# Kernel tuning notes

Measured on AMD Instinct MI355X. Metric: run time of the kernel, lower is better.

The kernel has to match this reference:

```python
import jax, jax.numpy as jnp
import numpy as np

GRAPH_SIZE = 100   # nodes per graph (hardcoded reshape in Net.call)
CH = 64            # self.channel
BN_EPS = 1e-3      # keras BatchNormalization default epsilon

N_GRAPHS = 4096
N_NODES = N_GRAPHS * GRAPH_SIZE      # 409600
DEG = 16
N_EDGES = N_NODES * DEG              # 6,553,600


def setup_inputs() -> dict:
    key = jax.random.key(0)
    ks = jax.random.split(key, 12)
    x = jax.random.normal(ks[0], (N_NODES, CH), dtype=jnp.float32)
    # Edges confined within each 100-node graph block (disjoint-union batch).
    receivers = jax.random.randint(ks[1], (N_EDGES,), 0, N_NODES, dtype=jnp.int32)
    block = (receivers // GRAPH_SIZE) * GRAPH_SIZE
    senders = block + jax.random.randint(ks[2], (N_EDGES,), 0, GRAPH_SIZE, dtype=jnp.int32)
    s = lambda fan_in: 1.0 / np.sqrt(fan_in)
    return {
        "x": x,
        "senders": senders,
        "receivers": receivers,
        "W1": jax.random.normal(ks[3], (CH, CH), dtype=jnp.float32) * s(CH),
        "b1": jnp.zeros((CH,), jnp.float32),
        "gamma": jnp.ones((CH,), jnp.float32),
        "beta": jnp.zeros((CH,), jnp.float32),
        "bn_mean": jnp.zeros((CH,), jnp.float32),
        "bn_var": jnp.ones((CH,), jnp.float32),
        "W_d1": jax.random.normal(ks[4], (GRAPH_SIZE * CH, 256), dtype=jnp.float32) * s(GRAPH_SIZE * CH),
        "b_d1": jnp.zeros((256,), jnp.float32),
        "W_d2": jax.random.normal(ks[5], (256, 128), dtype=jnp.float32) * s(256),
        "b_d2": jnp.zeros((128,), jnp.float32),
        "W_d3": jax.random.normal(ks[6], (128, 1), dtype=jnp.float32) * s(128),
        "b_d3": jnp.zeros((1,), jnp.float32),
    }


def reference(x, senders, receivers, W1, b1, gamma, beta, bn_mean, bn_var,
              W_d1, b_d1, W_d2, b_d2, W_d3, b_d3):
    n = x.shape[0]
    # GeneralConv(aggregate='sum'): sum neighbor features, then linear+BN+ELU.
    agg = jax.ops.segment_sum(x[senders], receivers, num_segments=n)  # [N, CH]
    h = agg @ W1 + b1
    h = (h - bn_mean) * (gamma * jax.lax.rsqrt(bn_var + BN_EPS)) + beta
    h = jax.nn.elu(h)
    # reshape [N, CH] -> [N/100, 100*CH] (reshape + Flatten fused)
    h = h.reshape(n // GRAPH_SIZE, GRAPH_SIZE * CH)
    h = jax.nn.relu(h @ W_d1 + b_d1)
    h = jax.nn.relu(h @ W_d2 + b_d2)
    # dropout is identity at inference
    return jax.nn.sigmoid(h @ W_d3 + b_d3)  # [B, 1]
```

## Files before the change

### kernel.cpp

```cpp
#include <hip/hip_runtime.h>
#include <cstdint>
#include <cstddef>

#define GRAPH_SIZE 100
#define N_GRAPHS 4096
#define N_NODES (N_GRAPHS * GRAPH_SIZE)
#define DEG 16
#define N_EDGES (N_NODES * DEG)
#define BN_EPS 1e-3f

#define NB1 1024
#define NPB 400
#define PCHUNK 12800
#define NPWG (N_EDGES / PCHUNK)
#define BSTRIDE 8192
#define ECAP 2304

__global__ __launch_bounds__(256) void count1_kernel(const int* __restrict__ recv,
                                                     unsigned* __restrict__ wg_hist) {
  __shared__ unsigned lh[NB1];
  int tid = threadIdx.x, w = blockIdx.x;
  for (int i = tid; i < NB1; i += 256) lh[i] = 0;
  __syncthreads();
  size_t base = (size_t)w * PCHUNK;
  for (int i = tid; i < PCHUNK; i += 256)
    atomicAdd(&lh[(unsigned)recv[base + i] / NPB], 1u);
  __syncthreads();
  for (int i = tid; i < NB1; i += 256) wg_hist[(size_t)w * NB1 + i] = lh[i];
}

__global__ __launch_bounds__(256) void scan_wg_kernel(unsigned* __restrict__ wg_hist,
                                                      unsigned* __restrict__ gtotal) {
  int b = blockIdx.x * 256 + threadIdx.x;
  unsigned run = 0;
  for (int w = 0; w < NPWG; w++) {
    size_t idx = (size_t)w * NB1 + b;
    unsigned c = wg_hist[idx];
    wg_hist[idx] = run;
    run += c;
  }
  gtotal[b] = run;
}

__global__ __launch_bounds__(256) void scan_bucket_kernel(const unsigned* __restrict__ gtotal,
                                                          unsigned* __restrict__ gbase) {
  __shared__ unsigned tmp[256];
  int tid = threadIdx.x;
  unsigned my[4], s4 = 0;
#pragma unroll
  for (int j = 0; j < 4; j++) { my[j] = gtotal[tid * 4 + j]; s4 += my[j]; }
  tmp[tid] = s4;
  __syncthreads();
  unsigned acc = s4;
  for (int d = 1; d < 256; d <<= 1) {
    unsigned t = (tid >= d) ? tmp[tid - d] : 0;
    __syncthreads();
    acc += t;
    tmp[tid] = acc;
    __syncthreads();
  }
  unsigned run = tmp[tid] - s4;
#pragma unroll
  for (int j = 0; j < 4; j++) { gbase[tid * 4 + j] = run; run += my[j]; }
}

__global__ __launch_bounds__(256) void partition1_kernel(const int* __restrict__ recv,
                                                         const int* __restrict__ send,
                                                         const unsigned* __restrict__ wg_hist,
                                                         const unsigned* __restrict__ gbase,
                                                         unsigned short* __restrict__ midrec) {
  __shared__ unsigned cur[NB1];
  __shared__ unsigned tmp[256];
  __shared__ unsigned stage[PCHUNK];
  int tid = threadIdx.x, w = blockIdx.x;
  size_t base = (size_t)w * PCHUNK;

  for (int i = tid; i < NB1; i += 256) cur[i] = 0;
  __syncthreads();
  for (int i = tid; i < PCHUNK; i += 256)
    atomicAdd(&cur[(unsigned)recv[base + i] / NPB], 1u);
  __syncthreads();

  unsigned my[4], s4 = 0;
#pragma unroll
  for (int j = 0; j < 4; j++) { my[j] = cur[tid * 4 + j]; s4 += my[j]; }
  tmp[tid] = s4;
  __syncthreads();
  unsigned acc = s4;
  for (int d = 1; d < 256; d <<= 1) {
    unsigned t = (tid >= d) ? tmp[tid - d] : 0;
    __syncthreads();
    acc += t;
    tmp[tid] = acc;
    __syncthreads();
  }
  unsigned run = tmp[tid] - s4;
#pragma unroll
  for (int j = 0; j < 4; j++) { cur[tid * 4 + j] = run; run += my[j]; }
  __syncthreads();

  for (int i = tid; i < PCHUNK; i += 256) {
    unsigned r = (unsigned)recv[base + i];
    unsigned s = (unsigned)send[base + i];
    unsigned b = r / NPB;
    unsigned rin = r - b * NPB;
    unsigned gib = rin / 100;
    unsigned rl = rin - gib * 100;
    unsigned sl = s - (s / 100) * 100;
    unsigned pos = atomicAdd(&cur[b], 1u);
    stage[pos] = (b << 16) | (gib << 14) | (sl << 7) | rl;
  }
  __syncthreads();

  const unsigned* wrow = wg_hist + (size_t)w * NB1;
  for (int p = tid; p < PCHUNK; p += 256) {
    unsigned rec = stage[p];
    unsigned b = rec >> 16;
    unsigned start = (b > 0) ? cur[b - 1] : 0;
    unsigned dest = gbase[b] + wrow[b] + ((unsigned)p - start);
    midrec[dest] = (unsigned short)(rec & 0xFFFFu);
  }
}

__global__ __launch_bounds__(256) void sort2_kernel(const unsigned short* __restrict__ midrec,
                                                    const unsigned* __restrict__ gtotal,
                                                    const unsigned* __restrict__ gbase,
                                                    unsigned short* __restrict__ sorted,
                                                    unsigned* __restrict__ noff) {
  __shared__ unsigned short smid[BSTRIDE];
  __shared__ unsigned short dst[BSTRIDE];
  __shared__ unsigned hist[512];
  __shared__ unsigned tmp[256];
  __shared__ unsigned s_ptot;
  int tid = threadIdx.x, b = blockIdx.x;
  unsigned cnt = gtotal[b];
  if (cnt > BSTRIDE) cnt = BSTRIDE;
  unsigned gb = gbase[b];

  for (unsigned i = tid; i < cnt; i += 256) smid[i] = midrec[gb + i];
  hist[tid] = 0; hist[256 + tid] = 0;
  {
    unsigned* d32 = (unsigned*)dst;
    for (int i = tid; i < BSTRIDE / 2; i += 256) d32[i] = 0x19001900u;
  }
  __syncthreads();

  for (unsigned i = tid; i < cnt; i += 256) {
    unsigned rec = smid[i];
    unsigned nib = (rec >> 14) * 100 + (rec & 127u);
    atomicAdd(&hist[nib], 1u);
  }
  __syncthreads();

  unsigned c0 = hist[2 * tid], c1 = hist[2 * tid + 1];
  unsigned p0 = (c0 + 3u) & ~3u, p1 = (c1 + 3u) & ~3u;
  unsigned s2 = p0 + p1;
  tmp[tid] = s2;
  __syncthreads();
  unsigned acc = s2;
  for (int d = 1; d < 256; d <<= 1) {
    unsigned t = (tid >= d) ? tmp[tid - d] : 0;
    __syncthreads();
    acc += t;
    tmp[tid] = acc;
    __syncthreads();
  }
  unsigned pb0 = acc - s2;
  unsigned pb1 = pb0 + p0;
  unsigned obase = (unsigned)b * BSTRIDE;
  int k0 = 2 * tid, k1 = 2 * tid + 1;
  if (k0 <= NPB) noff[(size_t)b * 401 + k0] = obase + pb0;
  if (k1 <= NPB) noff[(size_t)b * 401 + k1] = obase + pb1;
  if (k0 == NPB) s_ptot = pb0;
  __syncthreads();
  hist[k0] = pb0;
  hist[k1] = pb1;
  __syncthreads();

  for (unsigned i = tid; i < cnt; i += 256) {
    unsigned rec = smid[i];
    unsigned nib = (rec >> 14) * 100 + (rec & 127u);
    unsigned pos = atomicAdd(&hist[nib], 1u);
    if (pos < BSTRIDE) dst[pos] = (unsigned short)(((rec >> 7) & 127u) * 64u);
  }
  __syncthreads();

  unsigned ptot = s_ptot;
  if (ptot > BSTRIDE) ptot = BSTRIDE;
  unsigned* o32 = (unsigned*)sorted + (size_t)b * (BSTRIDE / 2);
  unsigned* d32 = (unsigned*)dst;
  for (unsigned i = tid; i < (ptot >> 1); i += 256) o32[i] = d32[i];
}

__global__ __launch_bounds__(256) void aggconv_kernel(
    const float* __restrict__ x, const unsigned* __restrict__ noff,
    const unsigned short* __restrict__ sorted,
    const float* __restrict__ W1, const float* __restrict__ b1,
    const float* __restrict__ gamma, const float* __restrict__ beta,
    const float* __restrict__ bn_mean, const float* __restrict__ bn_var,
    float* __restrict__ h) {
  __shared__ float xs[6464];
  __shared__ unsigned short es[ECAP];
  __shared__ unsigned nof[104];
  int tid = threadIdx.x, lane = tid & 63, wv = tid >> 6;
  int g = blockIdx.x;
  size_t gb64 = (size_t)g * 6400;

  const float4* xsrc = (const float4*)(x + gb64);
  float4* xd = (float4*)xs;
  for (int i = tid; i < 1600; i += 256) xd[i] = xsrc[i];
  if (tid < 64) xs[6400 + tid] = 0.f;

  int b = g >> 2, gib = g & 3;
  size_t base401 = (size_t)b * 401 + (size_t)gib * 100;
  unsigned gbeg = noff[base401];
  unsigned gend = noff[base401 + 100];
  unsigned ecnt = gend - gbeg;
  if (ecnt > ECAP) ecnt = ECAP;
  if (tid <= 100) nof[tid] = noff[base401 + tid] - gbeg;
  {
    const unsigned* s32 = (const unsigned*)sorted + (gbeg >> 1);
    unsigned* e32 = (unsigned*)es;
    for (unsigned i = tid; i < (ecnt >> 1); i += 256) e32[i] = s32[i];
  }
  __syncthreads();

  float accs[25];
#pragma unroll
  for (int J = 0; J < 25; J++) {
    int n = wv + 4 * J;
    unsigned e = nof[n], e1 = nof[n + 1];
    float acc = 0.f;
    for (; e < e1; e += 4) {
      unsigned long long v = *(const unsigned long long*)&es[e];
      acc += xs[((unsigned)v & 0xFFFFu) + lane];
      acc += xs[((unsigned)(v >> 16) & 0xFFFFu) + lane];
      acc += xs[((unsigned)(v >> 32) & 0xFFFFu) + lane];
      acc += xs[(unsigned)(v >> 48) + lane];
    }
    accs[J] = acc;
  }
  __syncthreads();
#pragma unroll
  for (int J = 0; J < 25; J++) xs[(wv + 4 * J) * 64 + lane] = accs[J];
  __syncthreads();

  float w[64];
#pragma unroll
  for (int i = 0; i < 64; i++) w[i] = W1[i * 64 + lane];
  float scale = gamma[lane] * rsqrtf(bn_var[lane] + BN_EPS);
  float mb = bn_mean[lane], bt = beta[lane], bias1 = b1[lane];

#pragma unroll
  for (int J = 0; J < 25; J++) {
    int n = wv + 4 * J;
    float hv = bias1;
#pragma unroll
    for (int q = 0; q < 16; q++) {
      float4 av = *(const float4*)&xs[n * 64 + q * 4];
      hv = fmaf(av.x, w[q * 4 + 0], hv);
      hv = fmaf(av.y, w[q * 4 + 1], hv);
      hv = fmaf(av.z, w[q * 4 + 2], hv);
      hv = fmaf(av.w, w[q * 4 + 3], hv);
    }
    hv = (hv - mb) * scale + bt;
    hv = (hv > 0.f) ? hv : expm1f(hv);
    h[gb64 + (size_t)n * 64 + lane] = hv;
  }
}

#define G2_K 6400
#define G2_SPLIT 8
#define G2_KSLICE (G2_K / G2_SPLIT)
__global__ __launch_bounds__(256) void gemm2_kernel(const float* __restrict__ A,
                                                    const float* __restrict__ B,
                                                    float* __restrict__ Cp) {
  __shared__ float As[16][68];
  __shared__ float Bs[16][256];
  int tid = threadIdx.x;
  int tx = tid & 31;
  int ty = tid >> 5;
  int bm = blockIdx.x * 64;
  int k0base = blockIdx.y * G2_KSLICE;

  float acc[8][8] = {};

  int lm = tid >> 2;
  int lk = (tid & 3) * 4;
  const float* Aptr = A + (size_t)(bm + lm) * G2_K + k0base + lk;
  const float* Bptr = B + (size_t)k0base * 256 + tid;

  float4 apre = *(const float4*)Aptr;
  float bpre[16];
#pragma unroll
  for (int r = 0; r < 16; r++) bpre[r] = Bptr[r * 256];

  const int NT = G2_KSLICE / 16;
  for (int kt = 0; kt < NT; kt++) {
    As[lk + 0][lm] = apre.x;
    As[lk + 1][lm] = apre.y;
    As[lk + 2][lm] = apre.z;
    As[lk + 3][lm] = apre.w;
#pragma unroll
    for (int r = 0; r < 16; r++) Bs[r][tid] = bpre[r];
    __syncthreads();

    if (kt + 1 < NT) {
      apre = *(const float4*)(Aptr + (kt + 1) * 16);
#pragma unroll
      for (int r = 0; r < 16; r++) bpre[r] = Bptr[((kt + 1) * 16 + r) * 256];
    }

#pragma unroll
    for (int kk = 0; kk < 16; kk++) {
      float4 aa = *(const float4*)&As[kk][ty * 8];
      float4 ab = *(const float4*)&As[kk][ty * 8 + 4];
      float a[8] = {aa.x, aa.y, aa.z, aa.w, ab.x, ab.y, ab.z, ab.w};
      float bf[8];
#pragma unroll
      for (int j = 0; j < 8; j++) bf[j] = Bs[kk][tx + 32 * j];
#pragma unroll
      for (int i = 0; i < 8; i++)
#pragma unroll
        for (int j = 0; j < 8; j++) acc[i][j] = fmaf(a[i], bf[j], acc[i][j]);
    }
    __syncthreads();
  }

  float* out = Cp + (size_t)blockIdx.y * N_GRAPHS * 256;
#pragma unroll
  for (int i = 0; i < 8; i++)
#pragma unroll
    for (int j = 0; j < 8; j++)
      out[(size_t)(bm + ty * 8 + i) * 256 + tx + 32 * j] = acc[i][j];
}

__global__ __launch_bounds__(256) void reduce_kernel(const float* __restrict__ Cp,
                                                     const float* __restrict__ bias,
                                                     float* __restrict__ out1) {
  int i = blockIdx.x * 256 + threadIdx.x;
  const size_t S = (size_t)N_GRAPHS * 256;
  float v = bias[i & 255];
#pragma unroll
  for (int s = 0; s < G2_SPLIT; s++) v += Cp[s * S + i];
  out1[i] = fmaxf(v, 0.f);
}

__global__ __launch_bounds__(256) void tail_kernel(const float* __restrict__ out1,
                                                   const float* __restrict__ Wd2,
                                                   const float* __restrict__ bd2,
                                                   const float* __restrict__ Wd3,
                                                   const float* __restrict__ bd3,
                                                   float* __restrict__ out) {
  int lane = threadIdx.x & 63;
  int wave = threadIdx.x >> 6;
  int row = blockIdx.x * 4 + wave;

  const float* in = out1 + (size_t)row * 256;
  float i0 = in[lane];
  float i1 = in[64 + lane];
  float i2 = in[128 + lane];
  float i3 = in[192 + lane];

  float a0 = bd2[lane];
  float a1 = bd2[64 + lane];
#pragma unroll
  for (int i = 0; i < 64; i++) {
    float v0 = __shfl(i0, i);
    a0 = fmaf(v0, Wd2[(i)*128 + lane], a0);
    a1 = fmaf(v0, Wd2[(i)*128 + 64 + lane], a1);
    float v1 = __shfl(i1, i);
    a0 = fmaf(v1, Wd2[(64 + i) * 128 + lane], a0);
    a1 = fmaf(v1, Wd2[(64 + i) * 128 + 64 + lane], a1);
    float v2 = __shfl(i2, i);
    a0 = fmaf(v2, Wd2[(128 + i) * 128 + lane], a0);
    a1 = fmaf(v2, Wd2[(128 + i) * 128 + 64 + lane], a1);
    float v3 = __shfl(i3, i);
    a0 = fmaf(v3, Wd2[(192 + i) * 128 + lane], a0);
    a1 = fmaf(v3, Wd2[(192 + i) * 128 + 64 + lane], a1);
  }
  a0 = fmaxf(a0, 0.f);
  a1 = fmaxf(a1, 0.f);
  float p = a0 * Wd3[lane] + a1 * Wd3[64 + lane];
#pragma unroll
  for (int m = 32; m >= 1; m >>= 1) p += __shfl_xor(p, m);
  if (lane == 0) out[row] = 1.f / (1.f + expf(-(p + bd3[0])));
}

extern "C" void kernel_launch(void* const* d_in, const int* in_sizes, int n_in,
                              void* d_out, int out_size, void* d_ws, size_t ws_size,
                              hipStream_t stream) {
  const float* x        = (const float*)d_in[0];
  const int*   senders  = (const int*)d_in[1];
  const int*   receivers= (const int*)d_in[2];
  const float* W1       = (const float*)d_in[3];
  const float* b1       = (const float*)d_in[4];
  const float* gamma    = (const float*)d_in[5];
  const float* beta     = (const float*)d_in[6];
  const float* bn_mean  = (const float*)d_in[7];
  const float* bn_var   = (const float*)d_in[8];
  const float* W_d1     = (const float*)d_in[9];
  const float* b_d1     = (const float*)d_in[10];
  const float* W_d2     = (const float*)d_in[11];
  const float* b_d2     = (const float*)d_in[12];
  const float* W_d3     = (const float*)d_in[13];
  const float* b_d3     = (const float*)d_in[14];
  float* out = (float*)d_out;

  char* ws = (char*)d_ws;
  float* h = (float*)ws;                 ws += (size_t)N_NODES * 64 * 4;
  char* regB = ws;                       ws += (size_t)NPWG * NB1 * 4;
  unsigned* wg_hist = (unsigned*)regB;
  unsigned* noff    = (unsigned*)regB;
  unsigned* gtotal  = (unsigned*)ws;     ws += NB1 * 4;
  unsigned* gbase   = (unsigned*)ws;     ws += NB1 * 4;
  char* regDE = ws;
  unsigned short* midrec = (unsigned short*)regDE;
  unsigned short* sorted = (unsigned short*)(regDE + (size_t)N_EDGES * 2);
  float* Cp   = (float*)regDE;
  float* out1 = (float*)(regDE + (size_t)G2_SPLIT * N_GRAPHS * 256 * 4);

  count1_kernel<<<NPWG, 256, 0, stream>>>(receivers, wg_hist);
  scan_wg_kernel<<<NB1 / 256, 256, 0, stream>>>(wg_hist, gtotal);
  scan_bucket_kernel<<<1, 256, 0, stream>>>(gtotal, gbase);
  partition1_kernel<<<NPWG, 256, 0, stream>>>(receivers, senders, wg_hist, gbase, midrec);
  sort2_kernel<<<NB1, 256, 0, stream>>>(midrec, gtotal, gbase, sorted, noff);
  aggconv_kernel<<<N_GRAPHS, 256, 0, stream>>>(x, noff, sorted, W1, b1,
                                               gamma, beta, bn_mean, bn_var, h);
  gemm2_kernel<<<dim3(N_GRAPHS / 64, G2_SPLIT), 256, 0, stream>>>(h, W_d1, Cp);
  reduce_kernel<<<(N_GRAPHS * 256) / 256, 256, 0, stream>>>(Cp, b_d1, out1);
  tail_kernel<<<N_GRAPHS / 4, 256, 0, stream>>>(out1, W_d2, b_d2, W_d3, b_d3, out);
}
```

Measured before the change: 627.9 us.

## Run dense-layer GEMM on bf16 MFMA with split hi/lo precision emulation

```diff
diff --git a/kernel.cpp b/kernel.cpp
--- a/kernel.cpp
+++ b/kernel.cpp
@@ -15,6 +15,18 @@
 #define NPWG (N_EDGES / PCHUNK)
 #define BSTRIDE 8192
 #define ECAP 2304
+
+typedef __attribute__((ext_vector_type(8))) unsigned short ushort8;
+typedef __attribute__((ext_vector_type(8))) short short8;
+typedef __attribute__((ext_vector_type(4))) float f32x4;
+
+__device__ __forceinline__ unsigned f2bf(float f) {
+  unsigned u = __float_as_uint(f);
+  return (u + 0x7FFFu + ((u >> 16) & 1u)) >> 16;
+}
+__device__ __forceinline__ float bf2f(unsigned h) {
+  return __uint_as_float(h << 16);
+}
 
 __global__ __launch_bounds__(256) void count1_kernel(const int* __restrict__ recv,
                                                      unsigned* __restrict__ wg_hist) {
@@ -198,7 +210,7 @@
     const float* __restrict__ W1, const float* __restrict__ b1,
     const float* __restrict__ gamma, const float* __restrict__ beta,
     const float* __restrict__ bn_mean, const float* __restrict__ bn_var,
-    float* __restrict__ h) {
+    unsigned short* __restrict__ h_hi, unsigned short* __restrict__ h_lo) {
   __shared__ float xs[6464];
   __shared__ unsigned short es[ECAP];
   __shared__ unsigned nof[104];
@@ -265,74 +277,135 @@
     }
     hv = (hv - mb) * scale + bt;
     hv = (hv > 0.f) ? hv : expm1f(hv);
-    h[gb64 + (size_t)n * 64 + lane] = hv;
-  }
-}
-
-#define G2_K 6400
+    unsigned hi = f2bf(hv);
+    unsigned lo = f2bf(hv - bf2f(hi));
+    size_t idx = gb64 + (size_t)n * 64 + lane;
+    h_hi[idx] = (unsigned short)hi;
+    h_lo[idx] = (unsigned short)lo;
+  }
+}
+
+__global__ __launch_bounds__(256) void wcvt_kernel(const float* __restrict__ W,
+                                                   unsigned short* __restrict__ Bhi,
+                                                   unsigned short* __restrict__ Blo) {
+  __shared__ float sm[64][65];
+  int tid = threadIdx.x;
+  int k0 = blockIdx.x * 64;
+  int n0 = blockIdx.y * 64;
+  for (int i = tid; i < 1024; i += 256) {
+    int r = i >> 4, c4 = i & 15;
+    float4 v = *(const float4*)&W[(size_t)(k0 + r) * 256 + n0 + c4 * 4];
+    sm[r][c4 * 4 + 0] = v.x; sm[r][c4 * 4 + 1] = v.y;
+    sm[r][c4 * 4 + 2] = v.z; sm[r][c4 * 4 + 3] = v.w;
+  }
+  __syncthreads();
+  for (int i = tid; i < 512; i += 256) {
+    int nn = i >> 3, kk = i & 7;
+    ushort8 hi, lo;
+#pragma unroll
+    for (int j = 0; j < 8; j++) {
+      float f = sm[kk * 8 + j][nn];
+      unsigned hb = f2bf(f);
+      hi[j] = (unsigned short)hb;
+      lo[j] = (unsigned short)f2bf(f - bf2f(hb));
+    }
+    size_t o = (size_t)(n0 + nn) * 6400 + k0 + kk * 8;
+    *(ushort8*)&Bhi[o] = hi;
+    *(ushort8*)&Blo[o] = lo;
+  }
+}
+
 #define G2_SPLIT 8
-#define G2_KSLICE (G2_K / G2_SPLIT)
-__global__ __launch_bounds__(256) void gemm2_kernel(const float* __restrict__ A,
-                                                    const float* __restrict__ B,
+#define G2_KSLICE 800
+#define G2_STEPS (G2_KSLICE / 32)
+__global__ __launch_bounds__(256) void gemm2_kernel(const unsigned short* __restrict__ Ahi,
+                                                    const unsigned short* __restrict__ Alo,
+                                                    const unsigned short* __restrict__ Bhi,
+                                                    const unsigned short* __restrict__ Blo,
                                                     float* __restrict__ Cp) {
-  __shared__ float As[16][68];
-  __shared__ float Bs[16][256];
+  __shared__ __align__(16) unsigned short As[2][64 * 40];
+  __shared__ __align__(16) unsigned short Bs[2][256 * 40];
   int tid = threadIdx.x;
-  int tx = tid & 31;
-  int ty = tid >> 5;
+  int w = tid >> 6, l = tid & 63;
   int bm = blockIdx.x * 64;
-  int k0base = blockIdx.y * G2_KSLICE;
-
-  float acc[8][8] = {};
-
-  int lm = tid >> 2;
-  int lk = (tid & 3) * 4;
-  const float* Aptr = A + (size_t)(bm + lm) * G2_K + k0base + lk;
-  const float* Bptr = B + (size_t)k0base * 256 + tid;
-
-  float4 apre = *(const float4*)Aptr;
-  float bpre[16];
-#pragma unroll
-  for (int r = 0; r < 16; r++) bpre[r] = Bptr[r * 256];
-
-  const int NT = G2_KSLICE / 16;
-  for (int kt = 0; kt < NT; kt++) {
-    As[lk + 0][lm] = apre.x;
-    As[lk + 1][lm] = apre.y;
-    As[lk + 2][lm] = apre.z;
-    As[lk + 3][lm] = apre.w;
-#pragma unroll
-    for (int r = 0; r < 16; r++) Bs[r][tid] = bpre[r];
-    __syncthreads();
-
-    if (kt + 1 < NT) {
-      apre = *(const float4*)(Aptr + (kt + 1) * 16);
-#pragma unroll
-      for (int r = 0; r < 16; r++) bpre[r] = Bptr[((kt + 1) * 16 + r) * 256];
-    }
-
-#pragma unroll
-    for (int kk = 0; kk < 16; kk++) {
-      float4 aa = *(const float4*)&As[kk][ty * 8];
-      float4 ab = *(const float4*)&As[kk][ty * 8 + 4];
-      float a[8] = {aa.x, aa.y, aa.z, aa.w, ab.x, ab.y, ab.z, ab.w};
-      float bf[8];
-#pragma unroll
-      for (int j = 0; j < 8; j++) bf[j] = Bs[kk][tx + 32 * j];
-#pragma unroll
-      for (int i = 0; i < 8; i++)
-#pragma unroll
-        for (int j = 0; j < 8; j++) acc[i][j] = fmaf(a[i], bf[j], acc[i][j]);
-    }
-    __syncthreads();
-  }
-
-  float* out = Cp + (size_t)blockIdx.y * N_GRAPHS * 256;
-#pragma unroll
-  for (int i = 0; i < 8; i++)
-#pragma unroll
-    for (int j = 0; j < 8; j++)
-      out[(size_t)(bm + ty * 8 + i) * 256 + tx + 32 * j] = acc[i][j];
+  int kslice = blockIdx.y * G2_KSLICE;
+
+  f32x4 acc[4][4];
+#pragma unroll
+  for (int i = 0; i < 4; i++)
+#pragma unroll
+    for (int j = 0; j < 4; j++) acc[i][j] = (f32x4){0.f, 0.f, 0.f, 0.f};
+
+  int arow = tid >> 2, akg = tid & 3;
+  const size_t abase = (size_t)(bm + arow) * 6400 + kslice + akg * 8;
+
+  ushort8 pa_hi, pa_lo, pb_hi[4], pb_lo[4];
+  pa_hi = *(const ushort8*)&Ahi[abase];
+  pa_lo = *(const ushort8*)&Alo[abase];
+#pragma unroll
+  for (int i = 0; i < 4; i++) {
+    int u = tid + 256 * i;
+    size_t bb = (size_t)(u >> 2) * 6400 + kslice + (u & 3) * 8;
+    pb_hi[i] = *(const ushort8*)&Bhi[bb];
+    pb_lo[i] = *(const ushort8*)&Blo[bb];
+  }
+
+  for (int step = 0; step < G2_STEPS; step++) {
+    __syncthreads();
+    *(ushort8*)&As[0][arow * 40 + akg * 8] = pa_hi;
+    *(ushort8*)&As[1][arow * 40 + akg * 8] = pa_lo;
+#pragma unroll
+    for (int i = 0; i < 4; i++) {
+      int u = tid + 256 * i;
+      *(ushort8*)&Bs[0][(u >> 2) * 40 + (u & 3) * 8] = pb_hi[i];
+      *(ushort8*)&Bs[1][(u >> 2) * 40 + (u & 3) * 8] = pb_lo[i];
+    }
+    __syncthreads();
+
+    if (step + 1 < G2_STEPS) {
+      size_t koff = (size_t)(step + 1) * 32;
+      pa_hi = *(const ushort8*)&Ahi[abase + koff];
+      pa_lo = *(const ushort8*)&Alo[abase + koff];
+#pragma unroll
+      for (int i = 0; i < 4; i++) {
+        int u = tid + 256 * i;
+        size_t bb = (size_t)(u >> 2) * 6400 + kslice + (u & 3) * 8 + koff;
+        pb_hi[i] = *(const ushort8*)&Bhi[bb];
+        pb_lo[i] = *(const ushort8*)&Blo[bb];
+      }
+    }
+
+    int kg8 = (l >> 4) * 8;
+    short8 a_hi[4], a_lo[4];
+#pragma unroll
+    for (int mf = 0; mf < 4; mf++) {
+      int r = mf * 16 + (l & 15);
+      a_hi[mf] = *(const short8*)&As[0][r * 40 + kg8];
+      a_lo[mf] = *(const short8*)&As[1][r * 40 + kg8];
+    }
+#pragma unroll
+    for (int nf = 0; nf < 4; nf++) {
+      int c = w * 64 + nf * 16 + (l & 15);
+      short8 b_hi = *(const short8*)&Bs[0][c * 40 + kg8];
+      short8 b_lo = *(const short8*)&Bs[1][c * 40 + kg8];
+#pragma unroll
+      for (int mf = 0; mf < 4; mf++) {
+        acc[mf][nf] = __builtin_amdgcn_mfma_f32_16x16x32_bf16(a_hi[mf], b_hi, acc[mf][nf], 0, 0, 0);
+        acc[mf][nf] = __builtin_amdgcn_mfma_f32_16x16x32_bf16(a_hi[mf], b_lo, acc[mf][nf], 0, 0, 0);
+        acc[mf][nf] = __builtin_amdgcn_mfma_f32_16x16x32_bf16(a_lo[mf], b_hi, acc[mf][nf], 0, 0, 0);
+      }
+    }
+  }
+
+  float* outp = Cp + (size_t)blockIdx.y * N_GRAPHS * 256;
+#pragma unroll
+  for (int mf = 0; mf < 4; mf++)
+#pragma unroll
+    for (int nf = 0; nf < 4; nf++)
+#pragma unroll
+      for (int r = 0; r < 4; r++)
+        outp[(size_t)(bm + mf * 16 + (l >> 4) * 4 + r) * 256 + w * 64 + nf * 16 + (l & 15)] =
+            acc[mf][nf][r];
 }
 
 __global__ __launch_bounds__(256) void reduce_kernel(const float* __restrict__ Cp,
@@ -408,12 +481,15 @@
   float* out = (float*)d_out;
 
   char* ws = (char*)d_ws;
-  float* h = (float*)ws;                 ws += (size_t)N_NODES * 64 * 4;
+  unsigned short* h_hi = (unsigned short*)ws; ws += (size_t)N_NODES * 64 * 2;
+  unsigned short* h_lo = (unsigned short*)ws; ws += (size_t)N_NODES * 64 * 2;
   char* regB = ws;                       ws += (size_t)NPWG * NB1 * 4;
   unsigned* wg_hist = (unsigned*)regB;
   unsigned* noff    = (unsigned*)regB;
   unsigned* gtotal  = (unsigned*)ws;     ws += NB1 * 4;
   unsigned* gbase   = (unsigned*)ws;     ws += NB1 * 4;
+  unsigned short* Bt_hi = (unsigned short*)ws; ws += (size_t)256 * 6400 * 2;
+  unsigned short* Bt_lo = (unsigned short*)ws; ws += (size_t)256 * 6400 * 2;
   char* regDE = ws;
   unsigned short* midrec = (unsigned short*)regDE;
   unsigned short* sorted = (unsigned short*)(regDE + (size_t)N_EDGES * 2);
@@ -425,9 +501,10 @@
   scan_bucket_kernel<<<1, 256, 0, stream>>>(gtotal, gbase);
   partition1_kernel<<<NPWG, 256, 0, stream>>>(receivers, senders, wg_hist, gbase, midrec);
   sort2_kernel<<<NB1, 256, 0, stream>>>(midrec, gtotal, gbase, sorted, noff);
+  wcvt_kernel<<<dim3(100, 4), 256, 0, stream>>>(W_d1, Bt_hi, Bt_lo);
   aggconv_kernel<<<N_GRAPHS, 256, 0, stream>>>(x, noff, sorted, W1, b1,
-                                               gamma, beta, bn_mean, bn_var, h);
-  gemm2_kernel<<<dim3(N_GRAPHS / 64, G2_SPLIT), 256, 0, stream>>>(h, W_d1, Cp);
+                                               gamma, beta, bn_mean, bn_var, h_hi, h_lo);
+  gemm2_kernel<<<dim3(N_GRAPHS / 64, G2_SPLIT), 256, 0, stream>>>(h_hi, h_lo, Bt_hi, Bt_lo, Cp);
   reduce_kernel<<<(N_GRAPHS * 256) / 256, 256, 0, stream>>>(Cp, b_d1, out1);
   tail_kernel<<<N_GRAPHS / 4, 256, 0, stream>>>(out1, W_d2, b_d2, W_d3, b_d3, out);
 }
```

Measured after the change: 514.4 us. -18.1%, faster.
